# Kernel optimization log

Hardware: AMD Instinct MI355X
Metric: run time of the kernel (lower is better)

## Reference

```python
import jax, jax.numpy as jnp
import numpy as np

N, C, H_IN, H_OUT = 4096, 256, 64, 128

def setup_inputs() -> dict:
    key = jax.random.key(0)
    kx, kw, kb = jax.random.split(key, 3)
    x = jax.random.normal(kx, (N, C, H_IN), dtype=jnp.float32)
    # Conv1d(groups=C) weight (C*h_out, 1, h_in) viewed as per-channel matrices (C, h_out, h_in)
    W = jax.random.normal(kw, (C, H_OUT, H_IN), dtype=jnp.float32) / np.sqrt(H_IN)
    b = jax.random.normal(kb, (C, H_OUT), dtype=jnp.float32) * 0.02
    return {"x": x, "W": W, "b": b}

def reference(x, W, b):
    # per-channel independent linear: out[n,c,o] = sum_i x[n,c,i] * W[c,o,i] + b[c,o]
    out = jnp.einsum('nci,coi->nco', x, W)
    return out + b[None, :, :]
```

## Files before the change

kernel.cpp:

```cpp
#include <hip/hip_runtime.h>

#define N_  4096
#define C_  256
#define HI_ 64
#define HO_ 128

typedef __attribute__((ext_vector_type(8))) short bf16x8;
typedef __attribute__((ext_vector_type(4))) float f32x4;

__device__ __forceinline__ short f2bf(float f) {
    union { float f; unsigned u; } v; v.f = f;
    unsigned r = v.u + 0x7fffu + ((v.u >> 16) & 1u);
    return (short)(r >> 16);
}

__device__ __forceinline__ bf16x8 cvt8(const float4& a, const float4& b) {
    bf16x8 t;
    t[0] = f2bf(a.x); t[1] = f2bf(a.y); t[2] = f2bf(a.z); t[3] = f2bf(a.w);
    t[4] = f2bf(b.x); t[5] = f2bf(b.y); t[6] = f2bf(b.z); t[7] = f2bf(b.w);
    return t;
}

__global__ __launch_bounds__(256) void dw_mfma(
    const float* __restrict__ x, const float* __restrict__ W,
    const float* __restrict__ bias, float* __restrict__ out)
{
    const int bx   = blockIdx.x;
    const int c    = bx & (C_ - 1);
    const int nseg = bx >> 8;
    const int tid  = threadIdx.x;
    const int wave = tid >> 6;
    const int lane = tid & 63;
    const int lr   = lane & 15;
    const int kq   = lane >> 4;

    bf16x8 bfrag[8][2];
    float  bv[8];
    const float* Wc = W + c * (HO_ * HI_);
    #pragma unroll
    for (int ot = 0; ot < 8; ++ot) {
        const int o = ot * 16 + lr;
        const float* wr = Wc + o * HI_ + kq * 8;
        #pragma unroll
        for (int kb = 0; kb < 2; ++kb) {
            const float4 w0 = *reinterpret_cast<const float4*>(wr + 32 * kb);
            const float4 w1 = *reinterpret_cast<const float4*>(wr + 32 * kb + 4);
            bfrag[ot][kb] = cvt8(w0, w1);
        }
        bv[ot] = bias[c * HO_ + o];
    }

    const int n_wave = nseg * 256 + wave * 64;

    #pragma unroll
    for (int ch = 0; ch < 4; ++ch) {
        const int n1 = n_wave + ch * 16;

        const float* xr = x + ((long)(n1 + lr) * C_ + c) * HI_ + kq * 8;
        bf16x8 afrag[2];
        #pragma unroll
        for (int kb = 0; kb < 2; ++kb) {
            const float4 a0 = *reinterpret_cast<const float4*>(xr + 32 * kb);
            const float4 a1 = *reinterpret_cast<const float4*>(xr + 32 * kb + 4);
            afrag[kb] = cvt8(a0, a1);
        }

        f32x4 acc[8];
        #pragma unroll
        for (int ot = 0; ot < 8; ++ot) acc[ot] = (f32x4){0.f, 0.f, 0.f, 0.f};
        #pragma unroll
        for (int kb = 0; kb < 2; ++kb) {
            #pragma unroll
            for (int ot = 0; ot < 8; ++ot) {
                acc[ot] = __builtin_amdgcn_mfma_f32_16x16x32_bf16(
                    afrag[kb], bfrag[ot][kb], acc[ot], 0, 0, 0);
            }
        }

        float* orow = out + ((long)(n1 + kq * 4) * C_ + c) * HO_ + lr;
        #pragma unroll
        for (int r = 0; r < 4; ++r) {
            #pragma unroll
            for (int ot = 0; ot < 8; ++ot) {
                orow[(long)r * (C_ * HO_) + ot * 16] = acc[ot][r] + bv[ot];
            }
        }
    }
}

extern "C" void kernel_launch(void* const* d_in, const int* in_sizes, int n_in,
                              void* d_out, int out_size, void* d_ws, size_t ws_size,
                              hipStream_t stream) {
    const float* x  = (const float*)d_in[0];
    const float* W  = (const float*)d_in[1];
    const float* b  = (const float*)d_in[2];
    float* out      = (float*)d_out;
    const int blocks = C_ * (N_ / 256);
    dw_mfma<<<dim3(blocks), dim3(256), 0, stream>>>(x, W, b, out);
}
```

Before: 735.7 us.

## Stage x, W and output through LDS for coalesced vector loads and stores

Weights are converted to bf16 once into a swizzled shared buffer instead of being held in registers. Input rows are loaded with coalesced float4 loads, prefetched one chunk ahead, and written to a per-wave swizzled LDS tile for MFMA fragment reads. Accumulators are transposed through a per-wave LDS buffer so output rows are written with contiguous float4 stores plus bias. This targets the poorly coalesced strided scalar stores and loads, at the cost of extra LDS traffic and shared-memory footprint that may reduce occupancy.

```diff
diff --git a/kernel.cpp b/kernel.cpp
--- a/kernel.cpp
+++ b/kernel.cpp
@@ -6,6 +6,7 @@
 #define HO_ 128
 
 typedef __attribute__((ext_vector_type(8))) short bf16x8;
+typedef __attribute__((ext_vector_type(4))) short bf16x4;
 typedef __attribute__((ext_vector_type(4))) float f32x4;
 
 __device__ __forceinline__ short f2bf(float f) {
@@ -14,17 +15,14 @@
     return (short)(r >> 16);
 }
 
-__device__ __forceinline__ bf16x8 cvt8(const float4& a, const float4& b) {
-    bf16x8 t;
-    t[0] = f2bf(a.x); t[1] = f2bf(a.y); t[2] = f2bf(a.z); t[3] = f2bf(a.w);
-    t[4] = f2bf(b.x); t[5] = f2bf(b.y); t[6] = f2bf(b.z); t[7] = f2bf(b.w);
-    return t;
-}
-
-__global__ __launch_bounds__(256) void dw_mfma(
+__global__ __launch_bounds__(256) void dw_v2(
     const float* __restrict__ x, const float* __restrict__ W,
     const float* __restrict__ bias, float* __restrict__ out)
 {
+    __shared__ __align__(16) short wbuf[128 * 64];
+    __shared__ __align__(16) short xbuf[4][16 * 64];
+    __shared__ __align__(16) float ebuf[4][8 * 132];
+
     const int bx   = blockIdx.x;
     const int c    = bx & (C_ - 1);
     const int nseg = bx >> 8;
@@ -34,36 +32,57 @@
     const int lr   = lane & 15;
     const int kq   = lane >> 4;
 
-    bf16x8 bfrag[8][2];
-    float  bv[8];
-    const float* Wc = W + c * (HO_ * HI_);
+    {
+        const float* Wc = W + c * (HO_ * HI_);
+        #pragma unroll
+        for (int j = 0; j < 8; ++j) {
+            const int row = j * 16 + (tid >> 4);
+            const int f   = tid & 15;
+            const float4 w = *reinterpret_cast<const float4*>(Wc + row * HI_ + f * 4);
+            bf16x4 v; v[0]=f2bf(w.x); v[1]=f2bf(w.y); v[2]=f2bf(w.z); v[3]=f2bf(w.w);
+            const int slot = f >> 1, low = f & 1;
+            *reinterpret_cast<bf16x4*>(
+                &wbuf[row * 64 + (((slot ^ (row & 7)) << 3) + low * 4)]) = v;
+        }
+    }
+    const float4 bv4 = *reinterpret_cast<const float4*>(bias + c * HO_ + (lane & 31) * 4);
+    __syncthreads();
+
+    short* xb = xbuf[wave];
+    float* eb = ebuf[wave];
+    const int  n_wave  = nseg * 256 + wave * 64;
+    const long xrow    = (long)C_ * HI_;
+    const float* xbase = x + ((long)n_wave * C_ + c) * HI_;
+
+    float4 pf[4];
     #pragma unroll
-    for (int ot = 0; ot < 8; ++ot) {
-        const int o = ot * 16 + lr;
-        const float* wr = Wc + o * HI_ + kq * 8;
-        #pragma unroll
-        for (int kb = 0; kb < 2; ++kb) {
-            const float4 w0 = *reinterpret_cast<const float4*>(wr + 32 * kb);
-            const float4 w1 = *reinterpret_cast<const float4*>(wr + 32 * kb + 4);
-            bfrag[ot][kb] = cvt8(w0, w1);
-        }
-        bv[ot] = bias[c * HO_ + o];
+    for (int j = 0; j < 4; ++j) {
+        const int R = j * 4 + (lane >> 4);
+        pf[j] = *reinterpret_cast<const float4*>(xbase + (long)R * xrow + (lane & 15) * 4);
     }
-
-    const int n_wave = nseg * 256 + wave * 64;
 
     #pragma unroll
     for (int ch = 0; ch < 4; ++ch) {
-        const int n1 = n_wave + ch * 16;
-
-        const float* xr = x + ((long)(n1 + lr) * C_ + c) * HI_ + kq * 8;
+        #pragma unroll
+        for (int j = 0; j < 4; ++j) {
+            const int R = j * 4 + (lane >> 4);
+            bf16x4 v; v[0]=f2bf(pf[j].x); v[1]=f2bf(pf[j].y); v[2]=f2bf(pf[j].z); v[3]=f2bf(pf[j].w);
+            const int f = lane & 15, slot = f >> 1, low = f & 1;
+            *reinterpret_cast<bf16x4*>(
+                &xb[R * 64 + (((slot ^ (R & 7)) << 3) + low * 4)]) = v;
+        }
+        if (ch < 3) {
+            #pragma unroll
+            for (int j = 0; j < 4; ++j) {
+                const int R = (ch + 1) * 16 + j * 4 + (lane >> 4);
+                pf[j] = *reinterpret_cast<const float4*>(xbase + (long)R * xrow + (lane & 15) * 4);
+            }
+        }
         bf16x8 afrag[2];
         #pragma unroll
-        for (int kb = 0; kb < 2; ++kb) {
-            const float4 a0 = *reinterpret_cast<const float4*>(xr + 32 * kb);
-            const float4 a1 = *reinterpret_cast<const float4*>(xr + 32 * kb + 4);
-            afrag[kb] = cvt8(a0, a1);
-        }
+        for (int kb = 0; kb < 2; ++kb)
+            afrag[kb] = *reinterpret_cast<bf16x8*>(
+                &xb[lr * 64 + (((kq + 4 * kb) ^ (lr & 7)) << 3)]);
 
         f32x4 acc[8];
         #pragma unroll
@@ -72,17 +91,33 @@
         for (int kb = 0; kb < 2; ++kb) {
             #pragma unroll
             for (int ot = 0; ot < 8; ++ot) {
+                const int o = ot * 16 + lr;
+                const bf16x8 bfrag = *reinterpret_cast<bf16x8*>(
+                    &wbuf[o * 64 + (((kq + 4 * kb) ^ (o & 7)) << 3)]);
                 acc[ot] = __builtin_amdgcn_mfma_f32_16x16x32_bf16(
-                    afrag[kb], bfrag[ot][kb], acc[ot], 0, 0, 0);
+                    afrag[kb], bfrag, acc[ot], 0, 0, 0);
             }
         }
 
-        float* orow = out + ((long)(n1 + kq * 4) * C_ + c) * HO_ + lr;
+        const int n1 = n_wave + ch * 16;
         #pragma unroll
-        for (int r = 0; r < 4; ++r) {
+        for (int h = 0; h < 2; ++h) {
             #pragma unroll
-            for (int ot = 0; ot < 8; ++ot) {
-                orow[(long)r * (C_ * HO_) + ot * 16] = acc[ot][r] + bv[ot];
+            for (int rr = 0; rr < 2; ++rr) {
+                const int r    = h * 2 + rr;
+                const int slot = kq * 2 + rr;
+                #pragma unroll
+                for (int ot = 0; ot < 8; ++ot)
+                    eb[slot * 132 + ot * 16 + lr] = acc[ot][r];
+            }
+            #pragma unroll
+            for (int j = 0; j < 4; ++j) {
+                const int slot = 2 * j + (lane >> 5);
+                const int row  = (slot >> 1) * 4 + h * 2 + (slot & 1);
+                float4 v = *reinterpret_cast<float4*>(&eb[slot * 132 + (lane & 31) * 4]);
+                v.x += bv4.x; v.y += bv4.y; v.z += bv4.z; v.w += bv4.w;
+                *reinterpret_cast<float4*>(
+                    out + ((long)(n1 + row) * C_ + c) * HO_ + (lane & 31) * 4) = v;
             }
         }
     }
@@ -96,5 +131,5 @@
     const float* b  = (const float*)d_in[2];
     float* out      = (float*)d_out;
     const int blocks = C_ * (N_ / 256);
-    dw_mfma<<<dim3(blocks), dim3(256), 0, stream>>>(x, W, b, out);
+    dw_v2<<<dim3(blocks), dim3(256), 0, stream>>>(x, W, b, out);
 }
```

Measured after the change: 719.1 us. -2.3%, faster.
